# Performance work log

Hardware: AMD Instinct MI355X
Metric: run time of the kernel (lower is better)

Reference implementation:

```python
import jax, jax.numpy as jnp
import numpy as np

B, L, D = 1, 4096, 1152
N, H = 16, 72            # num_heads, head_dim = d_model // num_heads
S = 64                   # num_patches_side = image_size // patch_size = 896 // 14
BASE = 100.0             # base_frequency for 2D RoPE
EPS = 1e-6


def _rmsnorm(t, scale):
    # t: [..., H]; Gemma-style zero-init scale -> multiply by (1 + scale)
    var = jnp.mean(t * t, axis=-1, keepdims=True)
    t = t * jax.lax.rsqrt(var + EPS)
    if scale is not None:
        t = t * (1.0 + scale)
    return t


def _rope_axis(t, pos):
    # t: [B, L, N, half]; pos: [B, L]. Split-half rotation with given base.
    half = t.shape[-1]
    freqs = BASE ** (-jnp.arange(0, half, 2, dtype=jnp.float32) * 2.0 / half)  # [half//2]
    ang = pos[:, :, None] * freqs                      # [B, L, half//2]
    cos = jnp.cos(ang)[:, :, None, :]
    sin = jnp.sin(ang)[:, :, None, :]
    t1, t2 = t[..., : half // 2], t[..., half // 2 :]
    return jnp.concatenate([t1 * cos - t2 * sin, t1 * sin + t2 * cos], axis=-1)


def _rope_2d(t, rows, cols):
    # first half of head_dim rotated by row position, second half by column position
    h2 = t.shape[-1] // 2
    return jnp.concatenate(
        [_rope_axis(t[..., :h2], rows), _rope_axis(t[..., h2:], cols)], axis=-1
    )


def setup_inputs() -> dict:
    key = jax.random.key(0)
    ks = jax.random.split(key, 5)
    s = 0.02
    return {
        "x": jax.random.normal(ks[0], (B, L, D), dtype=jnp.float32),
        "q_w": jax.random.normal(ks[1], (D, D), dtype=jnp.float32) * s,
        "q_b": jnp.zeros((D,), dtype=jnp.float32),
        "kv_w": jax.random.normal(ks[2], (D, 2 * D), dtype=jnp.float32) * s,
        "kv_b": jnp.zeros((2 * D,), dtype=jnp.float32),
        "o_w": jax.random.normal(ks[3], (D, D), dtype=jnp.float32) * s,
        "o_b": jnp.zeros((D,), dtype=jnp.float32),
        "q_scale": jnp.zeros((H,), dtype=jnp.float32),  # RMSNorm zero_init
        "k_scale": jnp.zeros((H,), dtype=jnp.float32),  # RMSNorm zero_init
    }


def reference(x, q_w, q_b, kv_w, kv_b, o_w, o_b, q_scale, k_scale):
    q = (x @ q_w + q_b).reshape(B, L, N, H)
    kv = (x @ kv_w + kv_b).reshape(B, L, 2, N, H)
    k, v = kv[:, :, 0], kv[:, :, 1]

    q = _rmsnorm(q, q_scale)
    k = _rmsnorm(k, k_scale)
    v = _rmsnorm(v, None)  # with_scale=False

    rows = jnp.repeat(jnp.arange(S, dtype=jnp.float32), S)[None, :L]  # [1, L]
    cols = jnp.tile(jnp.arange(S, dtype=jnp.float32), S)[None, :L]
    rows = jnp.broadcast_to(rows, (B, L))
    cols = jnp.broadcast_to(cols, (B, L))

    q = _rope_2d(q, rows, cols)  # scale = 1.0
    k = _rope_2d(k, rows, cols)

    attn = jnp.einsum("bqnh,bknh->bnqk", q, k)          # [B, N, L, L]
    attn = jax.nn.softmax(attn, axis=-1)
    out = jnp.einsum("bnqk,bknh->bqnh", attn, v).reshape(B, L, D)
    return out @ o_w + o_b
```

## Files before the change

### kernel.cpp

```cpp
#include <hip/hip_runtime.h>
#include <cstdint>
#include <cstddef>

#define LSEQ 4096
#define DMODEL 1152
#define NH 16
#define HD 72
#define HP96 96
#define HP80 80
#define NQKV 3456

typedef unsigned short u16;
typedef unsigned int u32;
typedef __attribute__((ext_vector_type(4))) float f32x4;
typedef __attribute__((ext_vector_type(4))) u32 u32x4;
typedef _Float16 f16x8 __attribute__((ext_vector_type(8), may_alias));
typedef unsigned short us8 __attribute__((ext_vector_type(8), may_alias));
typedef unsigned short us4 __attribute__((ext_vector_type(4), may_alias));

static __device__ __forceinline__ u16 f2h(float f) {
  _Float16 h = (_Float16)f;
  return __builtin_bit_cast(u16, h);
}
static __device__ __forceinline__ float h2f(u16 b) {
  return (float)__builtin_bit_cast(_Float16, b);
}

static __device__ __forceinline__ float fast_exp2(float x) {
#if __has_builtin(__builtin_amdgcn_exp2f)
  return __builtin_amdgcn_exp2f(x);
#else
  float r;
  asm("v_exp_f32 %0, %1" : "=v"(r) : "v"(x));
  return r;
#endif
}

__global__ void k_cvt_f16(const float* __restrict__ src, u16* __restrict__ dst, int n4) {
  int i = blockIdx.x * blockDim.x + threadIdx.x;
  int stride = gridDim.x * blockDim.x;
  for (; i < n4; i += stride) {
    float4 v = ((const float4*)src)[i];
    us4 o; o[0] = f2h(v.x); o[1] = f2h(v.y); o[2] = f2h(v.z); o[3] = f2h(v.w);
    ((us4*)dst)[i] = o;
  }
}

__global__ void k_transp_w(const float* __restrict__ src, u16* __restrict__ dst, int K, int N) {
  __shared__ float tile[32][33];
  int tx = threadIdx.x & 31, ty = threadIdx.x >> 5;
  int n0 = blockIdx.x * 32, k0 = blockIdx.y * 32;
#pragma unroll
  for (int j = 0; j < 4; ++j)
    tile[ty + j * 8][tx] = src[(size_t)(k0 + ty + j * 8) * N + n0 + tx];
  __syncthreads();
#pragma unroll
  for (int j = 0; j < 4; ++j)
    dst[(size_t)(n0 + ty + j * 8) * K + k0 + tx] = f2h(tile[tx][ty + j * 8]);
}

template <bool OUTF32>
__global__ __launch_bounds__(256) void k_gemm_bt(
    const u16* __restrict__ A, const u16* __restrict__ Bt,
    const float* __restrict__ bias, void* __restrict__ Cout,
    int M, int N, int K) {
  __shared__ __align__(16) u16 sA[128][40];
  __shared__ __align__(16) u16 sB[128][40];
  int t = threadIdx.x;
  int l = t & 63, w = t >> 6, lo = l & 15, hi = l >> 4;
  int m0 = blockIdx.y * 128, n0 = blockIdx.x * 128;
  int wm = (w >> 1) * 64, wn = (w & 1) * 64;
  int sr = t >> 1, sh = (t & 1) * 16;
  const u16* pa = A + (size_t)(m0 + sr) * K + sh;
  const u16* pb = Bt + (size_t)(n0 + sr) * K + sh;
  f32x4 acc[4][4] = {};
  us8 ra0 = *(const us8*)(pa), ra1 = *(const us8*)(pa + 8);
  us8 rb0 = *(const us8*)(pb), rb1 = *(const us8*)(pb + 8);
  int nk = K >> 5;
  for (int ks = 0; ks < nk; ++ks) {
    __syncthreads();
    *(us8*)&sA[sr][sh] = ra0; *(us8*)&sA[sr][sh + 8] = ra1;
    *(us8*)&sB[sr][sh] = rb0; *(us8*)&sB[sr][sh + 8] = rb1;
    if (ks + 1 < nk) {
      int off = (ks + 1) * 32;
      ra0 = *(const us8*)(pa + off); ra1 = *(const us8*)(pa + off + 8);
      rb0 = *(const us8*)(pb + off); rb1 = *(const us8*)(pb + off + 8);
    }
    __syncthreads();
    f16x8 af[4], bf[4];
#pragma unroll
    for (int mi = 0; mi < 4; ++mi) af[mi] = *(const f16x8*)&sA[wm + mi * 16 + lo][hi * 8];
#pragma unroll
    for (int ni = 0; ni < 4; ++ni) bf[ni] = *(const f16x8*)&sB[wn + ni * 16 + lo][hi * 8];
#pragma unroll
    for (int mi = 0; mi < 4; ++mi)
#pragma unroll
      for (int ni = 0; ni < 4; ++ni)
        acc[mi][ni] = __builtin_amdgcn_mfma_f32_16x16x32_f16(af[mi], bf[ni], acc[mi][ni], 0, 0, 0);
  }
#pragma unroll
  for (int mi = 0; mi < 4; ++mi)
#pragma unroll
    for (int ni = 0; ni < 4; ++ni) {
      int row = m0 + wm + mi * 16 + hi * 4;
      int col = n0 + wn + ni * 16 + lo;
      float bv = bias ? bias[col] : 0.0f;
#pragma unroll
      for (int rr = 0; rr < 4; ++rr) {
        float v = acc[mi][ni][rr] + bv;
        if (OUTF32) ((float*)Cout)[(size_t)(row + rr) * N + col] = v;
        else        ((u16*)Cout)[(size_t)(row + rr) * N + col] = f2h(v);
      }
    }
}

__global__ __launch_bounds__(256) void k_norm_rope(
    const u16* __restrict__ qkv,
    const float* __restrict__ q_b, const float* __restrict__ kv_b,
    const float* __restrict__ q_s, const float* __restrict__ k_s,
    u16* __restrict__ qp, u16* __restrict__ kp, u16* __restrict__ vn) {
  __shared__ float s_q[DMODEL], s_k[DMODEL], s_v[DMODEL];
  __shared__ float cs[4][18];
  int t = threadIdx.x;
  int tok = blockIdx.x;
  if (t < 36) {
    int i = t < 18 ? t : t - 18;
    float f = exp2f(-(float)i * (6.6438561897747247f / 9.0f));
    float pos = (t < 18) ? (float)(tok >> 6) : (float)(tok & 63);
    float s, c;
    sincosf(pos * f, &s, &c);
    if (t < 18) { cs[0][i] = c; cs[1][i] = s; }
    else        { cs[2][i] = c; cs[3][i] = s; }
  }
  const u16* rowp = qkv + (size_t)tok * NQKV;
  for (int idx = t; idx < DMODEL; idx += 256) {
    s_q[idx] = h2f(rowp[idx]) + q_b[idx];
    s_k[idx] = h2f(rowp[DMODEL + idx]) + kv_b[idx];
    s_v[idx] = h2f(rowp[2 * DMODEL + idx]) + kv_b[DMODEL + idx];
  }
  __syncthreads();
  int h = t >> 4, sub = t & 15;
  int base = h * HD;
  float aq = 0, ak = 0, av = 0;
#pragma unroll
  for (int j = 0; j < 5; ++j) {
    int idx = sub + 16 * j;
    if (idx < HD) {
      float a = s_q[base + idx], b = s_k[base + idx], c = s_v[base + idx];
      aq += a * a; ak += b * b; av += c * c;
    }
  }
#pragma unroll
  for (int m = 1; m <= 8; m <<= 1) {
    aq += __shfl_xor(aq, m, 64);
    ak += __shfl_xor(ak, m, 64);
    av += __shfl_xor(av, m, 64);
  }
  float rq = rsqrtf(aq / 72.f + 1e-6f);
  float rk = rsqrtf(ak / 72.f + 1e-6f);
  float rv = rsqrtf(av / 72.f + 1e-6f);
  size_t ob96 = ((size_t)h * LSEQ + tok) * HP96;
  size_t ob80 = ((size_t)h * LSEQ + tok) * HP80;
#pragma unroll
  for (int j = 0; j < 6; ++j) {
    int idx = sub + 16 * j;
    float oq = 0.f, ok = 0.f;
    if (idx < HD) {
      int sec = idx >= 36;
      int loc = idx - sec * 36;
      int i = loc >= 18 ? loc - 18 : loc;
      float c = cs[sec * 2 + 0][i], s = cs[sec * 2 + 1][i];
      int p1 = sec * 36 + i, p2 = p1 + 18;
      float q1 = s_q[base + p1] * rq * (1.f + q_s[p1]);
      float q2 = s_q[base + p2] * rq * (1.f + q_s[p2]);
      float k1 = s_k[base + p1] * rk * (1.f + k_s[p1]);
      float k2 = s_k[base + p2] * rk * (1.f + k_s[p2]);
      if (loc < 18) { oq = q1 * c - q2 * s; ok = k1 * c - k2 * s; }
      else          { oq = q1 * s + q2 * c; ok = k1 * s + k2 * c; }
    }
    qp[ob96 + idx] = f2h(oq);
    kp[ob96 + idx] = f2h(ok);
  }
#pragma unroll
  for (int j = 0; j < 5; ++j) {
    int idx = sub + 16 * j;
    float ov = (idx < HD) ? s_v[base + idx] * rv : (idx == 72 ? 1.0f : 0.f);
    vn[ob80 + idx] = f2h(ov);
  }
}

__global__ __launch_bounds__(256) void k_vfrag(const u16* __restrict__ vn, u16* __restrict__ vf) {
  __shared__ u16 tl[32][84];
  int head = blockIdx.y, kb = blockIdx.x;
  int t = threadIdx.x;
  const u16* src = vn + ((size_t)head * LSEQ + kb * 32) * HP80;
  for (int p = t; p < 32 * 20; p += 256) {
    int rr = p / 20, c4 = p % 20;
    *(us4*)&tl[rr][c4 * 4] = *(const us4*)(src + rr * HP80 + c4 * 4);
  }
  __syncthreads();
  u16* dst = vf + ((size_t)head * 128 + kb) * 2560;
  for (int u = t; u < 320; u += 256) {
    int ht = u >> 6, ll = u & 63, lo2 = ll & 15, hi2 = ll >> 4;
    us8 o;
#pragma unroll
    for (int j = 0; j < 8; ++j)
      o[j] = tl[(j >> 2) * 16 + hi2 * 4 + (j & 3)][ht * 16 + lo2];
    *(us8*)&dst[(size_t)u * 8] = o;
  }
}

__global__ __launch_bounds__(256, 2) void k_flash(
    const u16* __restrict__ qp, const u16* __restrict__ kp,
    const u16* __restrict__ vf, u16* __restrict__ pbuf, float2* __restrict__ dmb) {
  __shared__ __align__(16) u16 sK[64][104];
  int t = threadIdx.x;
  int l = t & 63, w = t >> 6, lo = l & 15, hi = l >> 4;
  int id = blockIdx.x, r = id >> 3;
  int half = r & 1, qb = (r >> 1) & 31, head = ((r >> 6) << 3) + (id & 7);
  const float L2E = 1.4426950408889634f;

  const u16* qbase = qp + ((size_t)head * LSEQ + qb * 128 + w * 32 + lo) * HP96 + hi * 8;
  f16x8 qf[2][3];
#pragma unroll
  for (int g = 0; g < 2; ++g)
#pragma unroll
    for (int c = 0; c < 3; ++c)
      qf[g][c] = *(const f16x8*)(qbase + g * 16 * HP96 + c * 32);

  f32x4 oacc[2][5] = {};
  float mrun[2];
#pragma unroll
  for (int g = 0; g < 2; ++g) mrun[g] = -__builtin_inff();

  int sr_ = t >> 2, sq4 = (t & 3) * 24;
  const u16* kptr = kp + ((size_t)head * LSEQ + half * 2048 + sr_) * HP96 + sq4;
  us8 kx0 = *(const us8*)(kptr), kx1 = *(const us8*)(kptr + 8), kx2 = *(const us8*)(kptr + 16);

  const u16* vptr = vf + ((size_t)head * 128 + half * 64) * 2560 + (size_t)l * 8;
  us8 vA[5], vB[5];
#pragma unroll
  for (int ht = 0; ht < 5; ++ht) vA[ht] = *(const us8*)(vptr + ht * 512);
  vptr += 2560;

  for (int kt = 0; kt < 32; ++kt) {
    __syncthreads();
    *(us8*)&sK[sr_][sq4] = kx0; *(us8*)&sK[sr_][sq4 + 8] = kx1; *(us8*)&sK[sr_][sq4 + 16] = kx2;
    if (kt < 31) {
      kx0 = *(const us8*)(kptr + 6144);
      kx1 = *(const us8*)(kptr + 6144 + 8);
      kx2 = *(const us8*)(kptr + 6144 + 16);
      kptr += 6144;
    }
    __syncthreads();
    f32x4 sacc[2][4] = {};
#pragma unroll
    for (int c = 0; c < 3; ++c)
#pragma unroll
      for (int nt = 0; nt < 4; ++nt) {
        f16x8 bk = *(const f16x8*)&sK[lo + 16 * nt][c * 32 + hi * 8];
#pragma unroll
        for (int g = 0; g < 2; ++g)
          sacc[g][nt] = __builtin_amdgcn_mfma_f32_16x16x32_f16(bk, qf[g][c], sacc[g][nt], 0, 0, 0);
      }
    float mt[2];
#pragma unroll
    for (int g = 0; g < 2; ++g) {
      float m = fmaxf(fmaxf(fmaxf(sacc[g][0][0], sacc[g][0][1]), sacc[g][0][2]), sacc[g][0][3]);
#pragma unroll
      for (int nt = 1; nt < 4; ++nt)
        m = fmaxf(m, fmaxf(fmaxf(fmaxf(sacc[g][nt][0], sacc[g][nt][1]), sacc[g][nt][2]), sacc[g][nt][3]));
      m = fmaxf(m, __shfl_xor(m, 16, 64));
      m = fmaxf(m, __shfl_xor(m, 32, 64));
      mt[g] = m;
    }
    bool need = (mt[0] > mrun[0] + 8.f) | (mt[1] > mrun[1] + 8.f);
    if (__any(need)) {
#pragma unroll
      for (int g = 0; g < 2; ++g) {
        float mn = fmaxf(mrun[g], mt[g]);
        float al = fast_exp2((mrun[g] - mn) * L2E);
        mrun[g] = mn;
#pragma unroll
        for (int ht = 0; ht < 5; ++ht)
#pragma unroll
          for (int rr = 0; rr < 4; ++rr) oacc[g][ht][rr] *= al;
      }
    }
#pragma unroll
    for (int kc = 0; kc < 2; ++kc) {
#pragma unroll
      for (int ht = 0; ht < 5; ++ht) vB[ht] = *(const us8*)(vptr + ht * 512);
      vptr += 2560;
#pragma unroll
      for (int g = 0; g < 2; ++g) {
        float nm = -mrun[g] * L2E;
        float p0[4], p1[4];
#pragma unroll
        for (int rr = 0; rr < 4; ++rr) {
          p0[rr] = fast_exp2(__builtin_fmaf(sacc[g][2 * kc][rr], L2E, nm));
          p1[rr] = fast_exp2(__builtin_fmaf(sacc[g][2 * kc + 1][rr], L2E, nm));
        }
        u32x4 pw = {__builtin_bit_cast(u32, __builtin_amdgcn_cvt_pkrtz(p0[0], p0[1])),
                    __builtin_bit_cast(u32, __builtin_amdgcn_cvt_pkrtz(p0[2], p0[3])),
                    __builtin_bit_cast(u32, __builtin_amdgcn_cvt_pkrtz(p1[0], p1[1])),
                    __builtin_bit_cast(u32, __builtin_amdgcn_cvt_pkrtz(p1[2], p1[3]))};
        f16x8 pb = __builtin_bit_cast(f16x8, pw);
#pragma unroll
        for (int ht = 0; ht < 5; ++ht)
          oacc[g][ht] = __builtin_amdgcn_mfma_f32_16x16x32_f16(
              __builtin_bit_cast(f16x8, vA[ht]), pb, oacc[g][ht], 0, 0, 0);
      }
#pragma unroll
      for (int ht = 0; ht < 5; ++ht) vA[ht] = vB[ht];
    }
  }
#pragma unroll
  for (int g = 0; g < 2; ++g) {
    float den = __shfl(oacc[g][4][0], lo + 32, 64);
    float inv = 1.f / den;
    int row = qb * 128 + w * 32 + g * 16 + lo;
    u16* orow = pbuf + ((size_t)half * LSEQ + row) * DMODEL + head * HD;
#pragma unroll
    for (int ht = 0; ht < 5; ++ht)
#pragma unroll
      for (int rr = 0; rr < 4; ++rr) {
        int h = 16 * ht + 4 * hi + rr;
        if (h < HD) orow[h] = f2h(oacc[g][ht][rr] * inv);
      }
    if (hi == 0) {
      float2 dm; dm.x = den; dm.y = mrun[g];
      dmb[((size_t)half * NH + head) * LSEQ + row] = dm;
    }
  }
}

__global__ __launch_bounds__(384) void k_combine(
    const u16* __restrict__ pbuf, const float2* __restrict__ dmb, u16* __restrict__ attb) {
  const float L2E = 1.4426950408889634f;
  int tok = blockIdx.x, t = threadIdx.x;
  for (int c = t; c < DMODEL; c += 384) {
    int head = c / HD;
    float2 dm0 = dmb[(size_t)head * LSEQ + tok];
    float2 dm1 = dmb[((size_t)NH + head) * LSEQ + tok];
    float M = fmaxf(dm0.y, dm1.y);
    float w0 = dm0.x * fast_exp2((dm0.y - M) * L2E);
    float w1 = dm1.x * fast_exp2((dm1.y - M) * L2E);
    float o0 = h2f(pbuf[(size_t)tok * DMODEL + c]);
    float o1 = h2f(pbuf[((size_t)LSEQ + tok) * DMODEL + c]);
    attb[(size_t)tok * DMODEL + c] = f2h((w0 * o0 + w1 * o1) / (w0 + w1));
  }
}

extern "C" void kernel_launch(void* const* d_in, const int* in_sizes, int n_in,
                              void* d_out, int out_size, void* d_ws, size_t ws_size,
                              hipStream_t stream) {
  const float* x    = (const float*)d_in[0];
  const float* q_w  = (const float*)d_in[1];
  const float* q_b  = (const float*)d_in[2];
  const float* kv_w = (const float*)d_in[3];
  const float* kv_b = (const float*)d_in[4];
  const float* o_w  = (const float*)d_in[5];
  const float* o_b  = (const float*)d_in[6];
  const float* q_s  = (const float*)d_in[7];
  const float* k_s  = (const float*)d_in[8];
  char* ws = (char*)d_ws;
  u16* xb   = (u16*)(ws + 0);
  u16* wT   = (u16*)(ws + 9437184);
  u16* oT   = (u16*)(ws + 17399808);
  u16* qkvb = (u16*)(ws + 20054016);
  u16* qp   = (u16*)(ws + 48365568);
  u16* kp   = (u16*)(ws + 60948480);
  u16* vn   = (u16*)(ws + 73531392);
  u16* vfb  = (u16*)(ws + 0);
  float2* dmb = (float2*)(ws + 10485760);
  u16* attb = (u16*)(ws + 20054016);
  u16* pbuf = (u16*)(ws + 29491200);

  k_cvt_f16<<<2048, 256, 0, stream>>>(x, xb, LSEQ * DMODEL / 4);
  k_transp_w<<<dim3(36, 36), 256, 0, stream>>>(q_w, wT, DMODEL, DMODEL);
  k_transp_w<<<dim3(72, 36), 256, 0, stream>>>(kv_w, wT + (size_t)DMODEL * DMODEL, DMODEL, 2 * DMODEL);
  k_transp_w<<<dim3(36, 36), 256, 0, stream>>>(o_w, oT, DMODEL, DMODEL);
  k_gemm_bt<false><<<dim3(27, 32), 256, 0, stream>>>(xb, wT, nullptr, qkvb, LSEQ, NQKV, DMODEL);
  k_norm_rope<<<LSEQ, 256, 0, stream>>>(qkvb, q_b, kv_b, q_s, k_s, qp, kp, vn);
  k_vfrag<<<dim3(128, 16), 256, 0, stream>>>(vn, vfb);
  k_flash<<<1024, 256, 0, stream>>>(qp, kp, vfb, pbuf, dmb);
  k_combine<<<LSEQ, 384, 0, stream>>>(pbuf, dmb, attb);
  k_gemm_bt<true><<<dim3(9, 32), 256, 0, stream>>>(attb, oT, o_b, (float*)d_out, LSEQ, DMODEL, DMODEL);
}
```

Before: 257.4 us.

## Use direct global-to-LDS loads in GEMM and streamline attention softmax loop

```diff
diff --git a/kernel.cpp b/kernel.cpp
--- a/kernel.cpp
+++ b/kernel.cpp
@@ -17,6 +17,15 @@
 typedef _Float16 f16x8 __attribute__((ext_vector_type(8), may_alias));
 typedef unsigned short us8 __attribute__((ext_vector_type(8), may_alias));
 typedef unsigned short us4 __attribute__((ext_vector_type(4), may_alias));
+
+#ifndef __has_builtin
+#define __has_builtin(x) 0
+#endif
+#if __has_builtin(__builtin_amdgcn_global_load_lds)
+#define HAS_GLL 1
+#else
+#define HAS_GLL 0
+#endif
 
 static __device__ __forceinline__ u16 f2h(float f) {
   _Float16 h = (_Float16)f;
@@ -36,6 +45,18 @@
 #endif
 }
 
+static __device__ __forceinline__ float max3f(float a, float b, float c) {
+  return fmaxf(fmaxf(a, b), c);
+}
+
+#if HAS_GLL
+static __device__ __forceinline__ void gll16(const u16* g, u16* s) {
+  __builtin_amdgcn_global_load_lds(
+      (const __attribute__((address_space(1))) u32*)g,
+      (__attribute__((address_space(3))) u32*)s, 16, 0, 0);
+}
+#endif
+
 __global__ void k_cvt_f16(const float* __restrict__ src, u16* __restrict__ dst, int n4) {
   int i = blockIdx.x * blockDim.x + threadIdx.x;
   int stride = gridDim.x * blockDim.x;
@@ -64,19 +85,49 @@
     const u16* __restrict__ A, const u16* __restrict__ Bt,
     const float* __restrict__ bias, void* __restrict__ Cout,
     int M, int N, int K) {
-  __shared__ __align__(16) u16 sA[128][40];
-  __shared__ __align__(16) u16 sB[128][40];
   int t = threadIdx.x;
   int l = t & 63, w = t >> 6, lo = l & 15, hi = l >> 4;
   int m0 = blockIdx.y * 128, n0 = blockIdx.x * 128;
   int wm = (w >> 1) * 64, wn = (w & 1) * 64;
+  f32x4 acc[4][4] = {};
+  int nk = K >> 5;
+#if HAS_GLL
+  __shared__ __align__(16) u16 sA[128][32];
+  __shared__ __align__(16) u16 sB[128][32];
+  int grow = w * 32 + (l >> 2);
+  int gcol = (l & 3) * 8;
+  const u16* pa = A + (size_t)(m0 + grow) * K + gcol;
+  const u16* pb = Bt + (size_t)(n0 + grow) * K + gcol;
+  u16* la = &sA[0][0] + w * 1024;
+  u16* lb = &sB[0][0] + w * 1024;
+  for (int ks = 0; ks < nk; ++ks) {
+    __syncthreads();
+    size_t ko = (size_t)ks * 32;
+#pragma unroll
+    for (int i = 0; i < 2; ++i) {
+      gll16(pa + (size_t)(i * 16) * K + ko, la + i * 512);
+      gll16(pb + (size_t)(i * 16) * K + ko, lb + i * 512);
+    }
+    __syncthreads();
+    f16x8 af[4], bf[4];
+#pragma unroll
+    for (int mi = 0; mi < 4; ++mi) af[mi] = *(const f16x8*)&sA[wm + mi * 16 + lo][hi * 8];
+#pragma unroll
+    for (int ni = 0; ni < 4; ++ni) bf[ni] = *(const f16x8*)&sB[wn + ni * 16 + lo][hi * 8];
+#pragma unroll
+    for (int mi = 0; mi < 4; ++mi)
+#pragma unroll
+      for (int ni = 0; ni < 4; ++ni)
+        acc[mi][ni] = __builtin_amdgcn_mfma_f32_16x16x32_f16(af[mi], bf[ni], acc[mi][ni], 0, 0, 0);
+  }
+#else
+  __shared__ __align__(16) u16 sA[128][40];
+  __shared__ __align__(16) u16 sB[128][40];
   int sr = t >> 1, sh = (t & 1) * 16;
   const u16* pa = A + (size_t)(m0 + sr) * K + sh;
   const u16* pb = Bt + (size_t)(n0 + sr) * K + sh;
-  f32x4 acc[4][4] = {};
   us8 ra0 = *(const us8*)(pa), ra1 = *(const us8*)(pa + 8);
   us8 rb0 = *(const us8*)(pb), rb1 = *(const us8*)(pb + 8);
-  int nk = K >> 5;
   for (int ks = 0; ks < nk; ++ks) {
     __syncthreads();
     *(us8*)&sA[sr][sh] = ra0; *(us8*)&sA[sr][sh + 8] = ra1;
@@ -98,6 +149,7 @@
       for (int ni = 0; ni < 4; ++ni)
         acc[mi][ni] = __builtin_amdgcn_mfma_f32_16x16x32_f16(af[mi], bf[ni], acc[mi][ni], 0, 0, 0);
   }
+#endif
 #pragma unroll
   for (int mi = 0; mi < 4; ++mi)
 #pragma unroll
@@ -266,10 +318,12 @@
     float mt[2];
 #pragma unroll
     for (int g = 0; g < 2; ++g) {
-      float m = fmaxf(fmaxf(fmaxf(sacc[g][0][0], sacc[g][0][1]), sacc[g][0][2]), sacc[g][0][3]);
-#pragma unroll
-      for (int nt = 1; nt < 4; ++nt)
-        m = fmaxf(m, fmaxf(fmaxf(fmaxf(sacc[g][nt][0], sacc[g][nt][1]), sacc[g][nt][2]), sacc[g][nt][3]));
+      float t0 = max3f(sacc[g][0][0], sacc[g][0][1], sacc[g][0][2]);
+      float t1 = max3f(sacc[g][0][3], sacc[g][1][0], sacc[g][1][1]);
+      float t2 = max3f(sacc[g][1][2], sacc[g][1][3], sacc[g][2][0]);
+      float t3 = max3f(sacc[g][2][1], sacc[g][2][2], sacc[g][2][3]);
+      float t4 = max3f(sacc[g][3][0], sacc[g][3][1], sacc[g][3][2]);
+      float m = fmaxf(max3f(t0, t1, t2), max3f(t3, t4, sacc[g][3][3]));
       m = fmaxf(m, __shfl_xor(m, 16, 64));
       m = fmaxf(m, __shfl_xor(m, 32, 64));
       mt[g] = m;
@@ -287,32 +341,50 @@
           for (int rr = 0; rr < 4; ++rr) oacc[g][ht][rr] *= al;
       }
     }
-#pragma unroll
-    for (int kc = 0; kc < 2; ++kc) {
-#pragma unroll
-      for (int ht = 0; ht < 5; ++ht) vB[ht] = *(const us8*)(vptr + ht * 512);
-      vptr += 2560;
-#pragma unroll
-      for (int g = 0; g < 2; ++g) {
-        float nm = -mrun[g] * L2E;
-        float p0[4], p1[4];
-#pragma unroll
-        for (int rr = 0; rr < 4; ++rr) {
-          p0[rr] = fast_exp2(__builtin_fmaf(sacc[g][2 * kc][rr], L2E, nm));
-          p1[rr] = fast_exp2(__builtin_fmaf(sacc[g][2 * kc + 1][rr], L2E, nm));
-        }
-        u32x4 pw = {__builtin_bit_cast(u32, __builtin_amdgcn_cvt_pkrtz(p0[0], p0[1])),
-                    __builtin_bit_cast(u32, __builtin_amdgcn_cvt_pkrtz(p0[2], p0[3])),
-                    __builtin_bit_cast(u32, __builtin_amdgcn_cvt_pkrtz(p1[0], p1[1])),
-                    __builtin_bit_cast(u32, __builtin_amdgcn_cvt_pkrtz(p1[2], p1[3]))};
-        f16x8 pb = __builtin_bit_cast(f16x8, pw);
-#pragma unroll
-        for (int ht = 0; ht < 5; ++ht)
-          oacc[g][ht] = __builtin_amdgcn_mfma_f32_16x16x32_f16(
-              __builtin_bit_cast(f16x8, vA[ht]), pb, oacc[g][ht], 0, 0, 0);
-      }
-#pragma unroll
-      for (int ht = 0; ht < 5; ++ht) vA[ht] = vB[ht];
+    float nm[2];
+#pragma unroll
+    for (int g = 0; g < 2; ++g) nm[g] = -mrun[g] * L2E;
+#pragma unroll
+    for (int ht = 0; ht < 5; ++ht) vB[ht] = *(const us8*)(vptr + ht * 512);
+    vptr += 2560;
+#pragma unroll
+    for (int g = 0; g < 2; ++g) {
+      float p0[4], p1[4];
+#pragma unroll
+      for (int rr = 0; rr < 4; ++rr) {
+        p0[rr] = fast_exp2(__builtin_fmaf(sacc[g][0][rr], L2E, nm[g]));
+        p1[rr] = fast_exp2(__builtin_fmaf(sacc[g][1][rr], L2E, nm[g]));
+      }
+      u32x4 pw = {__builtin_bit_cast(u32, __builtin_amdgcn_cvt_pkrtz(p0[0], p0[1])),
+                  __builtin_bit_cast(u32, __builtin_amdgcn_cvt_pkrtz(p0[2], p0[3])),
+                  __builtin_bit_cast(u32, __builtin_amdgcn_cvt_pkrtz(p1[0], p1[1])),
+                  __builtin_bit_cast(u32, __builtin_amdgcn_cvt_pkrtz(p1[2], p1[3]))};
+      f16x8 pb = __builtin_bit_cast(f16x8, pw);
+#pragma unroll
+      for (int ht = 0; ht < 5; ++ht)
+        oacc[g][ht] = __builtin_amdgcn_mfma_f32_16x16x32_f16(
+            __builtin_bit_cast(f16x8, vA[ht]), pb, oacc[g][ht], 0, 0, 0);
+    }
+#pragma unroll
+    for (int ht = 0; ht < 5; ++ht) vA[ht] = *(const us8*)(vptr + ht * 512);
+    vptr += 2560;
+#pragma unroll
+    for (int g = 0; g < 2; ++g) {
+      float p0[4], p1[4];
+#pragma unroll
+      for (int rr = 0; rr < 4; ++rr) {
+        p0[rr] = fast_exp2(__builtin_fmaf(sacc[g][2][rr], L2E, nm[g]));
+        p1[rr] = fast_exp2(__builtin_fmaf(sacc[g][3][rr], L2E, nm[g]));
+      }
+      u32x4 pw = {__builtin_bit_cast(u32, __builtin_amdgcn_cvt_pkrtz(p0[0], p0[1])),
+                  __builtin_bit_cast(u32, __builtin_amdgcn_cvt_pkrtz(p0[2], p0[3])),
+                  __builtin_bit_cast(u32, __builtin_amdgcn_cvt_pkrtz(p1[0], p1[1])),
+                  __builtin_bit_cast(u32, __builtin_amdgcn_cvt_pkrtz(p1[2], p1[3]))};
+      f16x8 pb = __builtin_bit_cast(f16x8, pw);
+#pragma unroll
+      for (int ht = 0; ht < 5; ++ht)
+        oacc[g][ht] = __builtin_amdgcn_mfma_f32_16x16x32_f16(
+            __builtin_bit_cast(f16x8, vB[ht]), pb, oacc[g][ht], 0, 0, 0);
     }
   }
 #pragma unroll
```

Measured after the change: 266.8 us. 1.04x slower.
